# Kernel tuning notes

Measured on AMD Instinct MI355X. Metric: run time of the kernel, lower is better.

Reference implementation:

```python
import jax, jax.numpy as jnp
import numpy as np

N = 50000
E = 800000
D_IN = 128
HEADS = 2
C = 64  # per-head channels = out_channels // heads


def setup_inputs() -> dict:
    key = jax.random.key(0)
    ks = jax.random.split(key, 10)
    scale = 1.0 / np.sqrt(D_IN)
    x = jax.random.normal(ks[0], (N, D_IN), dtype=jnp.float32)
    edge_index = jax.random.randint(ks[1], (2, E), 0, N, dtype=jnp.int64)
    Wq = jax.random.normal(ks[2], (D_IN, HEADS * C), dtype=jnp.float32) * scale
    Wk = jax.random.normal(ks[3], (D_IN, HEADS * C), dtype=jnp.float32) * scale
    Wv = jax.random.normal(ks[4], (D_IN, HEADS * C), dtype=jnp.float32) * scale
    Wskip = jax.random.normal(ks[5], (D_IN, HEADS * C), dtype=jnp.float32) * scale
    bq = jnp.zeros((HEADS * C,), dtype=jnp.float32)
    bk = jnp.zeros((HEADS * C,), dtype=jnp.float32)
    bv = jnp.zeros((HEADS * C,), dtype=jnp.float32)
    bskip = jnp.zeros((HEADS * C,), dtype=jnp.float32)
    return {"x": x, "edge_index": edge_index, "Wq": Wq, "bq": bq,
            "Wk": Wk, "bk": bk, "Wv": Wv, "bv": bv,
            "Wskip": Wskip, "bskip": bskip}


def reference(x, edge_index, Wq, bq, Wk, bk, Wv, bv, Wskip, bskip):
    # TGATLayer.forward == TransformerConv (eval mode, dropout inactive),
    # concat=True, root_weight=True, beta=False, no edge_attr.
    n = x.shape[0]
    src, dst = edge_index[0], edge_index[1]  # messages flow src -> dst
    q = (x @ Wq + bq).reshape(n, HEADS, C)  # [N,H,C] query of destination
    k = (x @ Wk + bk).reshape(n, HEADS, C)  # [N,H,C] key of source
    v = (x @ Wv + bv).reshape(n, HEADS, C)  # [N,H,C] value of source
    # per-edge attention logits: (q_i . k_j) / sqrt(C)   -> [E,H]
    alpha = (q[dst] * k[src]).sum(-1) * (1.0 / np.sqrt(C)).astype(np.float32)
    # segment softmax over incoming edges of each destination node
    m = jax.ops.segment_max(alpha, dst, num_segments=n)          # [N,H]
    a = jnp.exp(alpha - m[dst])                                  # [E,H]
    denom = jax.ops.segment_sum(a, dst, num_segments=n)          # [N,H]
    # weighted scatter-add of values
    agg = jax.ops.segment_sum(a[:, :, None] * v[src], dst, num_segments=n)  # [N,H,C]
    agg = agg / jnp.maximum(denom, 1e-16)[:, :, None]
    out = agg.reshape(n, HEADS * C) + (x @ Wskip + bskip)  # concat heads + root skip
    return out
```

## Files before the change

### kernel.cpp

```cpp
#include <hip/hip_runtime.h>
#include <hip/hip_bf16.h>

typedef __attribute__((ext_vector_type(4))) float f32x4;
typedef __attribute__((ext_vector_type(8))) short bf16x8;

#define AS1 __attribute__((address_space(1)))
#define AS3 __attribute__((address_space(3)))
#define CAP 64

static __device__ __forceinline__ ushort f2bf(float v) {
    __hip_bfloat16 h = __float2bfloat16(v);
    return *reinterpret_cast<ushort*>(&h);
}
static __device__ __forceinline__ float bl(uint u) { return __uint_as_float(u << 16); }
static __device__ __forceinline__ float bh(uint u) { return __uint_as_float(u & 0xffff0000u); }
static __device__ __forceinline__ float bhr(uint u) { return __uint_as_float(u); }

__global__ __launch_bounds__(256) void prep_kernel(
    const float* __restrict__ Wq, const float* __restrict__ bq,
    const float* __restrict__ Wk, const float* __restrict__ bk,
    const float* __restrict__ Wv, const float* __restrict__ bv,
    const float* __restrict__ Ws, const float* __restrict__ bs,
    ushort* __restrict__ WcatT, float* __restrict__ bcat,
    const int* __restrict__ ei, int* __restrict__ count,
    ushort* __restrict__ sorted_src, int E_, int nHist)
{
    if ((int)blockIdx.x < nHist) {
        int e = (int)blockIdx.x * 256 + threadIdx.x;
        if (e < E_) {
            int s = ei[e];
            int d = ei[E_ + e];
            int rk = atomicAdd(&count[d], 1);
            if (rk < CAP) sorted_src[(d << 6) + rk] = (ushort)s;
        }
        return;
    }
    int id = ((int)blockIdx.x - nHist) * 256 + threadIdx.x;
    int r = id >> 7, k = id & 127;
    int which, c;
    if (r < 128)      { which = 0; c = r; }
    else if (r < 384) { int j = r - 128; which = ((j & 3) < 2) ? 1 : 2;
                        c = ((j >> 2) << 1) + (j & 1); }
    else              { which = 3; c = r - 384; }
    const float* W = (which == 0) ? Wq : (which == 1) ? Wk : (which == 2) ? Wv : Ws;
    WcatT[(size_t)r * 128 + k] = f2bf(W[(size_t)k * 128 + c]);
    if (k == 0) {
        const float* b = (which == 0) ? bq : (which == 1) ? bk : (which == 2) ? bv : bs;
        bcat[r] = b[c];
    }
}

__global__ __launch_bounds__(256) void qkvs_mfma(
    const float* __restrict__ x, const ushort* __restrict__ WcatT,
    const float* __restrict__ bcat, ushort* __restrict__ yb, int n)
{
    __shared__ ushort smA[16384];

    const int t    = threadIdx.x;
    const int lane = t & 63;
    const int w    = t >> 6;
    const int wm   = w >> 1, wn = w & 1;
    const int row0 = blockIdx.x * 128;

    #pragma unroll
    for (int i = 0; i < 8; ++i) {
        int L = i * 256 + t;
        int r = L >> 4, ck = L & 15;
        int gr = min(row0 + r, n - 1);
        const float* gp = x + (size_t)gr * 128 + ck * 8;
        f32x4 lo = *reinterpret_cast<const f32x4*>(gp);
        f32x4 hi = *reinterpret_cast<const f32x4*>(gp + 4);
        uint4 o;
        o.x = (uint)f2bf(lo[0]) | ((uint)f2bf(lo[1]) << 16);
        o.y = (uint)f2bf(lo[2]) | ((uint)f2bf(lo[3]) << 16);
        o.z = (uint)f2bf(hi[0]) | ((uint)f2bf(hi[1]) << 16);
        o.w = (uint)f2bf(hi[2]) | ((uint)f2bf(hi[3]) << 16);
        *reinterpret_cast<uint4*>(smA + (size_t)r * 128 + ((ck ^ (r & 7)) << 3)) = o;
    }
    __syncthreads();

    #pragma unroll
    for (int ct = 0; ct < 4; ++ct) {
        f32x4 acc[4][4];
        #pragma unroll
        for (int i = 0; i < 4; ++i)
            #pragma unroll
            for (int j = 0; j < 4; ++j) acc[i][j] = (f32x4)(0.f);

        #pragma unroll
        for (int kb = 0; kb < 4; ++kb) {
            bf16x8 a[4], b[4];
            #pragma unroll
            for (int cn = 0; cn < 4; ++cn) {
                int wcol = ct * 128 + wn * 64 + cn * 16 + (lane & 15);
                b[cn] = *reinterpret_cast<const bf16x8*>(
                    WcatT + (size_t)wcol * 128 + kb * 32 + (lane >> 4) * 8);
            }
            #pragma unroll
            for (int rm = 0; rm < 4; ++rm) {
                int r  = wm * 64 + rm * 16 + (lane & 15);
                int ck = (kb * 4 + (lane >> 4)) ^ (r & 7);
                a[rm] = *reinterpret_cast<const bf16x8*>(smA + (size_t)r * 128 + ck * 8);
            }
            #pragma unroll
            for (int rm = 0; rm < 4; ++rm)
                #pragma unroll
                for (int cn = 0; cn < 4; ++cn)
                    acc[rm][cn] = __builtin_amdgcn_mfma_f32_16x16x32_bf16(
                        b[cn], a[rm], acc[rm][cn], 0, 0, 0);
        }

        #pragma unroll
        for (int rm = 0; rm < 4; ++rm) {
            int gr = row0 + wm * 64 + rm * 16 + (lane & 15);
            if (gr < n) {
                #pragma unroll
                for (int cn = 0; cn < 4; ++cn) {
                    int nb = wn * 64 + cn * 16 + (lane >> 4) * 4;
                    f32x4 bb = *reinterpret_cast<const f32x4*>(bcat + ct * 128 + nb);
                    f32x4 v  = acc[rm][cn];
                    uint2 o;
                    o.x = (uint)f2bf(v[0] + bb[0]) | ((uint)f2bf(v[1] + bb[1]) << 16);
                    o.y = (uint)f2bf(v[2] + bb[2]) | ((uint)f2bf(v[3] + bb[3]) << 16);
                    *reinterpret_cast<uint2*>(yb + (size_t)gr * 512 + ct * 128 + nb) = o;
                }
            }
        }
    }
}

static __device__ __forceinline__ float dotp(const float q[8], uint4 A, uint4 B) {
    return q[0]*bl(A.x) + q[1]*bhr(A.x) + q[2]*bl(A.z) + q[3]*bhr(A.z)
         + q[4]*bl(B.x) + q[5]*bhr(B.x) + q[6]*bl(B.z) + q[7]*bhr(B.z);
}
static __device__ __forceinline__ void accum(float (&acc)[8], float& den,
                                             float a, uint4 A, uint4 B) {
    den += a;
    acc[0] += a*bl(A.y); acc[1] += a*bhr(A.y); acc[2] += a*bl(A.w); acc[3] += a*bhr(A.w);
    acc[4] += a*bl(B.y); acc[5] += a*bhr(B.y); acc[6] += a*bl(B.w); acc[7] += a*bhr(B.w);
}

__global__ __launch_bounds__(256) void node_agg(
    const uint* __restrict__ yb32, const int* __restrict__ count,
    const ushort* __restrict__ sorted_src, float* __restrict__ out, int n)
{
    const int node = blockIdx.x * 4 + (threadIdx.x >> 6);
    const int lane = threadIdx.x & 63;
    if (node >= n) return;
    const int g  = lane >> 4;
    const int il = lane & 15;

    const uint* row = yb32 + (size_t)node * 256;
    const uint4 qv = *reinterpret_cast<const uint4*>(row + 4 * il);
    float q[8] = { bl(qv.x)*0.125f, bh(qv.x)*0.125f, bl(qv.y)*0.125f, bh(qv.y)*0.125f,
                   bl(qv.z)*0.125f, bh(qv.z)*0.125f, bl(qv.w)*0.125f, bh(qv.w)*0.125f };

    const int deg = min(count[node], CAP);
    const ushort* sp = sorted_src + ((size_t)node << 6);

    float acc[8] = {0.f,0.f,0.f,0.f,0.f,0.f,0.f,0.f};
    float den = 0.f;

    int e = 0;
    for (; e + 8 <= deg; e += 8) {
        const int sA = sp[e + g], sB = sp[e + 4 + g];
        const uint* pa = yb32 + (size_t)sA * 256 + 64 + 8 * il;
        const uint* pb = yb32 + (size_t)sB * 256 + 64 + 8 * il;
        uint4 Aa = *reinterpret_cast<const uint4*>(pa);
        uint4 Ba = *reinterpret_cast<const uint4*>(pa + 4);
        uint4 Ab = *reinterpret_cast<const uint4*>(pb);
        uint4 Bb = *reinterpret_cast<const uint4*>(pb + 4);
        float p1 = dotp(q, Aa, Ba);
        float p2 = dotp(q, Ab, Bb);
        p1 += __shfl_xor(p1, 1, 64);  p2 += __shfl_xor(p2, 1, 64);
        p1 += __shfl_xor(p1, 2, 64);  p2 += __shfl_xor(p2, 2, 64);
        p1 += __shfl_xor(p1, 4, 64);  p2 += __shfl_xor(p2, 4, 64);
        float a1 = __expf(p1), a2 = __expf(p2);
        accum(acc, den, a1, Aa, Ba);
        accum(acc, den, a2, Ab, Bb);
    }
    for (; e < deg; e += 4) {
        const int idx = e + g;
        const bool act = idx < deg;
        const int s = sp[act ? idx : deg - 1];
        const uint* pa = yb32 + (size_t)s * 256 + 64 + 8 * il;
        uint4 A = *reinterpret_cast<const uint4*>(pa);
        uint4 B = *reinterpret_cast<const uint4*>(pa + 4);
        float p = dotp(q, A, B);
        p += __shfl_xor(p, 1, 64);
        p += __shfl_xor(p, 2, 64);
        p += __shfl_xor(p, 4, 64);
        float a = act ? __expf(p) : 0.f;
        accum(acc, den, a, A, B);
    }

    #pragma unroll
    for (int j = 0; j < 8; ++j) {
        acc[j] += __shfl_xor(acc[j], 16, 64);
        acc[j] += __shfl_xor(acc[j], 32, 64);
    }
    den += __shfl_xor(den, 16, 64);
    den += __shfl_xor(den, 32, 64);

    if (lane < 16) {
        const float inv = 1.f / fmaxf(den, 1e-16f);
        const uint4 sv = *reinterpret_cast<const uint4*>(row + 192 + 4 * il);
        f32x4 o0, o1;
        o0[0] = acc[0]*inv + bl(sv.x);  o0[1] = acc[1]*inv + bh(sv.x);
        o0[2] = acc[2]*inv + bl(sv.y);  o0[3] = acc[3]*inv + bh(sv.y);
        o1[0] = acc[4]*inv + bl(sv.z);  o1[1] = acc[5]*inv + bh(sv.z);
        o1[2] = acc[6]*inv + bl(sv.w);  o1[3] = acc[7]*inv + bh(sv.w);
        float* op = out + (size_t)node * 128 + 8 * il;
        *reinterpret_cast<f32x4*>(op)     = o0;
        *reinterpret_cast<f32x4*>(op + 4) = o1;
    }
}

extern "C" void kernel_launch(void* const* d_in, const int* in_sizes, int n_in,
                              void* d_out, int out_size, void* d_ws, size_t ws_size,
                              hipStream_t stream) {
    const float* x  = (const float*)d_in[0];
    const int*   ei = (const int*)d_in[1];
    const float* Wq = (const float*)d_in[2];
    const float* bq = (const float*)d_in[3];
    const float* Wk = (const float*)d_in[4];
    const float* bk = (const float*)d_in[5];
    const float* Wv = (const float*)d_in[6];
    const float* bv = (const float*)d_in[7];
    const float* Ws = (const float*)d_in[8];
    const float* bs = (const float*)d_in[9];

    const int N = in_sizes[0] / 128;
    const int E = in_sizes[1] / 2;

    ushort* yb    = (ushort*)d_ws;
    ushort* WcatT = yb + (size_t)N * 512;
    float*  bcat  = (float*)(WcatT + 512 * 128);
    int*    count = (int*)(bcat + 512);
    ushort* sorted_src = (ushort*)(count + N);
    float* out      = (float*)d_out;

    hipMemsetAsync(count, 0, (size_t)N * sizeof(int), stream);

    const int nHist = (E + 255) / 256;
    prep_kernel<<<nHist + 256, 256, 0, stream>>>(
        Wq, bq, Wk, bk, Wv, bv, Ws, bs, WcatT, bcat, ei, count, sorted_src, E, nHist);

    qkvs_mfma<<<(N + 127) / 128, 256, 0, stream>>>(x, WcatT, bcat, yb, N);

    node_agg<<<(N + 3) / 4, 256, 0, stream>>>((const uint*)yb, count, sorted_src, out, N);
}
```

Before: 149.7 us.

## Split projection output into KV and Q/skip buffers; software-pipeline gather loop

The projection kernel now writes interleaved K/V rows into a compact 256-element buffer and Q plus skip into a separate buffer, instead of one 512-wide row per node. The gathered K/V rows become 512 bytes, so source-node gathers touch fewer cache lines and pages and the working set shrinks. The aggregation loop is also restructured to prefetch the next 4-edge group while computing the current one, replacing the 8-edge unroll with a one-stage software pipeline. The new loop has less explicit memory-level parallelism per iteration than the previous two-group unroll.

```diff
diff --git a/kernel.cpp b/kernel.cpp
--- a/kernel.cpp
+++ b/kernel.cpp
@@ -52,7 +52,8 @@
 
 __global__ __launch_bounds__(256) void qkvs_mfma(
     const float* __restrict__ x, const ushort* __restrict__ WcatT,
-    const float* __restrict__ bcat, ushort* __restrict__ yb, int n)
+    const float* __restrict__ bcat, ushort* __restrict__ kvb,
+    ushort* __restrict__ qs, int n)
 {
     __shared__ ushort smA[16384];
 
@@ -110,6 +111,8 @@
                         b[cn], a[rm], acc[rm][cn], 0, 0, 0);
         }
 
+        ushort* dst  = (ct == 0 || ct == 3) ? qs : kvb;
+        int     cofs = (ct == 2 || ct == 3) ? 128 : 0;
         #pragma unroll
         for (int rm = 0; rm < 4; ++rm) {
             int gr = row0 + wm * 64 + rm * 16 + (lane & 15);
@@ -122,7 +125,7 @@
                     uint2 o;
                     o.x = (uint)f2bf(v[0] + bb[0]) | ((uint)f2bf(v[1] + bb[1]) << 16);
                     o.y = (uint)f2bf(v[2] + bb[2]) | ((uint)f2bf(v[3] + bb[3]) << 16);
-                    *reinterpret_cast<uint2*>(yb + (size_t)gr * 512 + ct * 128 + nb) = o;
+                    *reinterpret_cast<uint2*>(dst + (size_t)gr * 256 + cofs + nb) = o;
                 }
             }
         }
@@ -141,8 +144,9 @@
 }
 
 __global__ __launch_bounds__(256) void node_agg(
-    const uint* __restrict__ yb32, const int* __restrict__ count,
-    const ushort* __restrict__ sorted_src, float* __restrict__ out, int n)
+    const uint* __restrict__ kv32, const uint* __restrict__ qs32,
+    const int* __restrict__ count, const ushort* __restrict__ sorted_src,
+    float* __restrict__ out, int n)
 {
     const int node = blockIdx.x * 4 + (threadIdx.x >> 6);
     const int lane = threadIdx.x & 63;
@@ -150,8 +154,8 @@
     const int g  = lane >> 4;
     const int il = lane & 15;
 
-    const uint* row = yb32 + (size_t)node * 256;
-    const uint4 qv = *reinterpret_cast<const uint4*>(row + 4 * il);
+    const uint* qrow = qs32 + (size_t)node * 128;
+    const uint4 qv = *reinterpret_cast<const uint4*>(qrow + 4 * il);
     float q[8] = { bl(qv.x)*0.125f, bh(qv.x)*0.125f, bl(qv.y)*0.125f, bh(qv.y)*0.125f,
                    bl(qv.z)*0.125f, bh(qv.z)*0.125f, bl(qv.w)*0.125f, bh(qv.w)*0.125f };
 
@@ -161,37 +165,37 @@
     float acc[8] = {0.f,0.f,0.f,0.f,0.f,0.f,0.f,0.f};
     float den = 0.f;
 
-    int e = 0;
-    for (; e + 8 <= deg; e += 8) {
-        const int sA = sp[e + g], sB = sp[e + 4 + g];
-        const uint* pa = yb32 + (size_t)sA * 256 + 64 + 8 * il;
-        const uint* pb = yb32 + (size_t)sB * 256 + 64 + 8 * il;
-        uint4 Aa = *reinterpret_cast<const uint4*>(pa);
-        uint4 Ba = *reinterpret_cast<const uint4*>(pa + 4);
-        uint4 Ab = *reinterpret_cast<const uint4*>(pb);
-        uint4 Bb = *reinterpret_cast<const uint4*>(pb + 4);
-        float p1 = dotp(q, Aa, Ba);
-        float p2 = dotp(q, Ab, Bb);
-        p1 += __shfl_xor(p1, 1, 64);  p2 += __shfl_xor(p2, 1, 64);
-        p1 += __shfl_xor(p1, 2, 64);  p2 += __shfl_xor(p2, 2, 64);
-        p1 += __shfl_xor(p1, 4, 64);  p2 += __shfl_xor(p2, 4, 64);
-        float a1 = __expf(p1), a2 = __expf(p2);
-        accum(acc, den, a1, Aa, Ba);
-        accum(acc, den, a2, Ab, Bb);
-    }
-    for (; e < deg; e += 4) {
-        const int idx = e + g;
-        const bool act = idx < deg;
-        const int s = sp[act ? idx : deg - 1];
-        const uint* pa = yb32 + (size_t)s * 256 + 64 + 8 * il;
-        uint4 A = *reinterpret_cast<const uint4*>(pa);
-        uint4 B = *reinterpret_cast<const uint4*>(pa + 4);
-        float p = dotp(q, A, B);
-        p += __shfl_xor(p, 1, 64);
-        p += __shfl_xor(p, 2, 64);
-        p += __shfl_xor(p, 4, 64);
-        float a = act ? __expf(p) : 0.f;
-        accum(acc, den, a, A, B);
+    const int nq = (deg + 3) >> 2;
+    if (nq > 0) {
+        bool act0 = g < deg;
+        int  s0   = sp[act0 ? g : 0];
+        const uint* p0 = kv32 + (size_t)s0 * 128 + 8 * il;
+        uint4 A0 = *reinterpret_cast<const uint4*>(p0);
+        uint4 B0 = *reinterpret_cast<const uint4*>(p0 + 4);
+
+        for (int qd = 1; qd < nq; ++qd) {
+            int  idx  = qd * 4 + g;
+            bool act1 = idx < deg;
+            int  s1   = sp[act1 ? idx : 0];
+            const uint* p1 = kv32 + (size_t)s1 * 128 + 8 * il;
+            uint4 A1 = *reinterpret_cast<const uint4*>(p1);
+            uint4 B1 = *reinterpret_cast<const uint4*>(p1 + 4);
+
+            float pd = dotp(q, A0, B0);
+            pd += __shfl_xor(pd, 1, 64);
+            pd += __shfl_xor(pd, 2, 64);
+            pd += __shfl_xor(pd, 4, 64);
+            float a = act0 ? __expf(pd) : 0.f;
+            accum(acc, den, a, A0, B0);
+
+            A0 = A1; B0 = B1; act0 = act1;
+        }
+        float pd = dotp(q, A0, B0);
+        pd += __shfl_xor(pd, 1, 64);
+        pd += __shfl_xor(pd, 2, 64);
+        pd += __shfl_xor(pd, 4, 64);
+        float a = act0 ? __expf(pd) : 0.f;
+        accum(acc, den, a, A0, B0);
     }
 
     #pragma unroll
@@ -204,7 +208,7 @@
 
     if (lane < 16) {
         const float inv = 1.f / fmaxf(den, 1e-16f);
-        const uint4 sv = *reinterpret_cast<const uint4*>(row + 192 + 4 * il);
+        const uint4 sv = *reinterpret_cast<const uint4*>(qrow + 64 + 4 * il);
         f32x4 o0, o1;
         o0[0] = acc[0]*inv + bl(sv.x);  o0[1] = acc[1]*inv + bh(sv.x);
         o0[2] = acc[2]*inv + bl(sv.y);  o0[3] = acc[3]*inv + bh(sv.y);
@@ -233,8 +237,9 @@
     const int N = in_sizes[0] / 128;
     const int E = in_sizes[1] / 2;
 
-    ushort* yb    = (ushort*)d_ws;
-    ushort* WcatT = yb + (size_t)N * 512;
+    ushort* kvb   = (ushort*)d_ws;
+    ushort* qs    = kvb + (size_t)N * 256;
+    ushort* WcatT = qs + (size_t)N * 256;
     float*  bcat  = (float*)(WcatT + 512 * 128);
     int*    count = (int*)(bcat + 512);
     ushort* sorted_src = (ushort*)(count + N);
@@ -246,7 +251,8 @@
     prep_kernel<<<nHist + 256, 256, 0, stream>>>(
         Wq, bq, Wk, bk, Wv, bv, Ws, bs, WcatT, bcat, ei, count, sorted_src, E, nHist);
 
-    qkvs_mfma<<<(N + 127) / 128, 256, 0, stream>>>(x, WcatT, bcat, yb, N);
-
-    node_agg<<<(N + 3) / 4, 256, 0, stream>>>((const uint*)yb, count, sorted_src, out, N);
-}
+    qkvs_mfma<<<(N + 127) / 128, 256, 0, stream>>>(x, WcatT, bcat, kvb, qs, N);
+
+    node_agg<<<(N + 3) / 4, 256, 0, stream>>>(
+        (const uint*)kvb, (const uint*)qs, count, sorted_src, out, N);
+}
```

New measurement: 147.2 us. About the same (-1.7%).
